# Performance work log

Measured on AMD Instinct MI355X. Metric: run time of the kernel, lower is better.

The kernel has to match this reference:

```python
import jax, jax.numpy as jnp
import numpy as np

H, D = 4, 64              # heads, per-head channels
NT, NC, NF = 20000, 200000, 40000  # table / column / fk_node counts
E_HC, E_BT, E_IS, E_PT = 200000, 200000, 80000, 80000


def _gatv2(x_src, x_dst, src, dst, Wl, Wr, att, b, n_dst):
    """PyG GATv2Conv (concat=True, negative_slope=0.2, no self loops)."""
    xl = (x_src @ Wl).reshape(-1, H, D)              # [Ns,H,D]
    xr = (x_dst @ Wr).reshape(-1, H, D)              # [Nd,H,D]
    e = jax.nn.leaky_relu(xl[src] + xr[dst], 0.2)    # [E,H,D]
    logit = jnp.einsum('ehd,hd->eh', e, att)         # [E,H]
    m = jax.ops.segment_max(logit, dst, num_segments=n_dst)
    z = jnp.exp(logit - m[dst])
    den = jax.ops.segment_sum(z, dst, num_segments=n_dst)
    alpha = z / den[dst]                             # softmax per dst node
    msg = xl[src] * alpha[:, :, None]                # [E,H,D]
    out = jax.ops.segment_sum(msg, dst, num_segments=n_dst)
    return out.reshape(n_dst, H * D) + b


def setup_inputs() -> dict:
    key = jax.random.key(0)
    ks = jax.random.split(key, 24)
    Fin, Fh, Fo = 256, H * D, 256
    f = lambda k, s: jax.random.normal(k, s, jnp.float32) * 0.05
    ri = lambda k, n, hi: jax.random.randint(k, (n,), 0, hi, jnp.int32)
    return dict(
        x_table=jax.random.normal(ks[0], (NT, Fin), jnp.float32),
        x_column=jax.random.normal(ks[1], (NC, Fin), jnp.float32),
        x_fk=jax.random.normal(ks[2], (NF, Fin), jnp.float32),
        lin_w=f(ks[3], (3, Fin, D)), lin_b=f(ks[4], (3, D)),
        out_w=f(ks[5], (3, Fh, Fo)), out_b=f(ks[6], (3, Fo)),
        Wl0=f(ks[7], (4, D, Fh)), Wr0=f(ks[8], (4, D, Fh)),
        att0=f(ks[9], (4, H, D)), b0=f(ks[10], (4, Fh)),
        Wl1=f(ks[11], (4, Fh, Fh)), Wr1=f(ks[12], (4, Fh, Fh)),
        att1=f(ks[13], (4, H, D)), b1=f(ks[14], (4, Fh)),
        src_hc=ri(ks[15], E_HC, NT), dst_hc=ri(ks[16], E_HC, NC),
        src_bt=ri(ks[17], E_BT, NC), dst_bt=ri(ks[18], E_BT, NT),
        src_is=ri(ks[19], E_IS, NC), dst_is=ri(ks[20], E_IS, NF),
        src_pt=ri(ks[21], E_PT, NF), dst_pt=ri(ks[22], E_PT, NC),
    )


def reference(x_table, x_column, x_fk, lin_w, lin_b, out_w, out_b,
              Wl0, Wr0, att0, b0, Wl1, Wr1, att1, b1,
              src_hc, dst_hc, src_bt, dst_bt, src_is, dst_is, src_pt, dst_pt):
    # per-type input projection + leaky_relu (slope 0.01)
    xt = jax.nn.leaky_relu(x_table @ lin_w[0] + lin_b[0], 0.01)
    xc = jax.nn.leaky_relu(x_column @ lin_w[1] + lin_b[1], 0.01)
    xf = jax.nn.leaky_relu(x_fk @ lin_w[2] + lin_b[2], 0.01)
    for Wl, Wr, att, b in ((Wl0, Wr0, att0, b0), (Wl1, Wr1, att1, b1)):
        o_hc = _gatv2(xt, xc, src_hc, dst_hc, Wl[0], Wr[0], att[0], b[0], NC)
        o_bt = _gatv2(xc, xt, src_bt, dst_bt, Wl[1], Wr[1], att[1], b[1], NT)
        o_is = _gatv2(xc, xf, src_is, dst_is, Wl[2], Wr[2], att[2], b[2], NF)
        o_pt = _gatv2(xf, xc, src_pt, dst_pt, Wl[3], Wr[3], att[3], b[3], NC)
        xt = jax.nn.elu(o_bt)                  # single edge type -> mean = itself
        xc = jax.nn.elu(0.5 * (o_hc + o_pt))   # HeteroConv aggr='mean'
        xf = jax.nn.elu(o_is)
    return (xt @ out_w[0] + out_b[0],
            xc @ out_w[1] + out_b[1],
            xf @ out_w[2] + out_b[2])
```

## Files before the change

### kernel.cpp

```cpp
#include <hip/hip_runtime.h>
#include <stdint.h>

typedef unsigned short ushort_t;
typedef unsigned int uint32;

#define NT 20000
#define NC 200000
#define NF 40000
#define E_HC 200000
#define E_BT 200000
#define E_IS 80000
#define E_PT 80000
#define FDIM 256
#define NHEAD 4
#define DHEAD 64

typedef _Float16 __attribute__((ext_vector_type(8))) half8;
typedef __attribute__((ext_vector_type(4))) float f32x4;

__device__ __forceinline__ ushort_t f2h(float f) {
    _Float16 h = (_Float16)f;
    ushort_t v;
    __builtin_memcpy(&v, &h, 2);
    return v;
}
__device__ __forceinline__ float h2f_u(ushort_t v) {
    _Float16 h;
    __builtin_memcpy(&h, &v, 2);
    return (float)h;
}
__device__ __forceinline__ float hlo(uint32 u) { return h2f_u((ushort_t)(u & 0xffffu)); }
__device__ __forceinline__ float hhi(uint32 u) { return h2f_u((ushort_t)(u >> 16)); }
__device__ __forceinline__ float finclamp(float v) {
    return fminf(fmaxf(v, -1e30f), 1e30f);
}

union U16x8 { ushort_t u[8]; uint4 q; };

__global__ void pack_layer_k(const float* __restrict__ Wl, const float* __restrict__ Wr,
                             ushort_t* __restrict__ ct, ushort_t* __restrict__ cc,
                             ushort_t* __restrict__ cf, int K) {
    int i = blockIdx.x * 256 + threadIdx.x;
    int per = K * 256;
    if (i >= 8 * per) return;
    int s = i / per, r = i - s * per;
    int k = r >> 8, n = r & 255;
    const float* src; ushort_t* dst; int col;
    switch (s) {
        case 0: src = Wl + 0 * per; dst = ct; col = n;        break;
        case 1: src = Wr + 1 * per; dst = ct; col = 256 + n;  break;
        case 2: src = Wr + 0 * per; dst = cc; col = n;        break;
        case 3: src = Wl + 1 * per; dst = cc; col = 256 + n;  break;
        case 4: src = Wl + 2 * per; dst = cc; col = 512 + n;  break;
        case 5: src = Wr + 3 * per; dst = cc; col = 768 + n;  break;
        case 6: src = Wr + 2 * per; dst = cf; col = n;        break;
        default: src = Wl + 3 * per; dst = cf; col = 256 + n; break;
    }
    dst[(size_t)col * K + k] = f2h(src[(size_t)k * 256 + n]);
}

__global__ void pack_out_k(const float* __restrict__ W, ushort_t* __restrict__ Wt) {
    int i = blockIdx.x * 256 + threadIdx.x;
    if (i >= 3 * 65536) return;
    int t = i >> 16, r = i & 65535;
    int k = r >> 8, n = r & 255;
    Wt[(size_t)t * 65536 + n * 256 + k] = f2h(W[(size_t)t * 65536 + k * 256 + n]);
}

__global__ void pack_lin_k(const float* __restrict__ W, ushort_t* __restrict__ Wt) {
    int i = blockIdx.x * 256 + threadIdx.x;
    if (i >= 3 * 16384) return;
    int t = i >> 14, r = i & 16383;
    int k = r >> 6, n = r & 63;
    Wt[(size_t)t * 16384 + n * 256 + k] = f2h(W[(size_t)t * 16384 + k * 64 + n]);
}

template<int CT>
__global__ __launch_bounds__(256) void gemm_mfma_k(
    const ushort_t* __restrict__ A, const ushort_t* __restrict__ Wt,
    const float* __restrict__ bias, void* __restrict__ Cv,
    int M, int N, int K)
{
    __shared__ __align__(16) ushort_t As[128][32];
    __shared__ __align__(16) ushort_t Bs[128][32];
    const int t = threadIdx.x;
    const int lane = t & 63;
    const int w = t >> 6;
    const int wr = (w >> 1) * 64, wc = (w & 1) * 64;
    const int m0 = blockIdx.x * 128;
    const int n0 = blockIdx.y * 128;
    const int lm = lane & 15, g = lane >> 4;

    f32x4 acc[4][4];
#pragma unroll
    for (int mi = 0; mi < 4; mi++)
#pragma unroll
        for (int ni = 0; ni < 4; ni++) acc[mi][ni] = (f32x4){0.f, 0.f, 0.f, 0.f};

    const int sr = t >> 1;
    const int ss = (t & 1) * 2;
    const int sw = (sr >> 1) & 3;

    for (int k0 = 0; k0 < K; k0 += 32) {
        {
            int row = m0 + sr;
            uint4 q0 = make_uint4(0u, 0u, 0u, 0u), q1 = q0;
            if (row < M) {
                const uint4* p = reinterpret_cast<const uint4*>(
                    A + (size_t)row * K + k0 + ss * 8);
                q0 = p[0]; q1 = p[1];
            }
            *reinterpret_cast<uint4*>(&As[sr][((ss + 0) ^ sw) * 8]) = q0;
            *reinterpret_cast<uint4*>(&As[sr][((ss + 1) ^ sw) * 8]) = q1;
        }
        {
            const uint4* p = reinterpret_cast<const uint4*>(
                Wt + (size_t)(n0 + sr) * K + k0 + ss * 8);
            uint4 q0 = p[0], q1 = p[1];
            *reinterpret_cast<uint4*>(&Bs[sr][((ss + 0) ^ sw) * 8]) = q0;
            *reinterpret_cast<uint4*>(&Bs[sr][((ss + 1) ^ sw) * 8]) = q1;
        }
        __syncthreads();
        half8 af[4], bf[4];
#pragma unroll
        for (int mi = 0; mi < 4; mi++) {
            int row = wr + mi * 16 + lm;
            af[mi] = *reinterpret_cast<const half8*>(
                &As[row][(g ^ ((row >> 1) & 3)) * 8]);
        }
#pragma unroll
        for (int ni = 0; ni < 4; ni++) {
            int row = wc + ni * 16 + lm;
            bf[ni] = *reinterpret_cast<const half8*>(
                &Bs[row][(g ^ ((row >> 1) & 3)) * 8]);
        }
#pragma unroll
        for (int mi = 0; mi < 4; mi++)
#pragma unroll
            for (int ni = 0; ni < 4; ni++)
                acc[mi][ni] = __builtin_amdgcn_mfma_f32_16x16x32_f16(
                    af[mi], bf[ni], acc[mi][ni], 0, 0, 0);
        __syncthreads();
    }

#pragma unroll
    for (int mi = 0; mi < 4; mi++) {
#pragma unroll
        for (int j = 0; j < 4; j++) {
            int row = m0 + wr + mi * 16 + g * 4 + j;
            if (row >= M) continue;
#pragma unroll
            for (int ni = 0; ni < 4; ni++) {
                int col = n0 + wc + ni * 16 + lm;
                float v = acc[mi][ni][j];
                if (bias) v += bias[col];
                v = finclamp(v);
                if (CT == 0) {
                    ((float*)Cv)[(size_t)row * N + col] = v;
                } else {
                    ((ushort_t*)Cv)[(size_t)row * N + col] = f2h(v);
                }
            }
        }
    }
}

__global__ __launch_bounds__(256) void gemm_in_k(
    const float* __restrict__ A, const ushort_t* __restrict__ Wt,
    const float* __restrict__ bias, ushort_t* __restrict__ C, int M, int K)
{
    __shared__ __align__(16) ushort_t As[128][32];
    __shared__ __align__(16) ushort_t Bs[64][32];
    const int t = threadIdx.x;
    const int lane = t & 63;
    const int w = t >> 6;
    const int m0 = blockIdx.x * 128;
    const int lm = lane & 15, g = lane >> 4;

    f32x4 acc[2][4];
#pragma unroll
    for (int mi = 0; mi < 2; mi++)
#pragma unroll
        for (int ni = 0; ni < 4; ni++) acc[mi][ni] = (f32x4){0.f, 0.f, 0.f, 0.f};

    const int sr = t >> 1;
    const int ss = (t & 1) * 2;
    const int sw = (sr >> 1) & 3;
    const int br = t >> 2;
    const int bs = t & 3;
    const int bw = (br >> 1) & 3;

    for (int k0 = 0; k0 < K; k0 += 32) {
        {
            int row = m0 + sr;
            U16x8 a, b;
            if (row < M) {
                const float4* p = reinterpret_cast<const float4*>(
                    A + (size_t)row * K + k0 + (t & 1) * 16);
                float4 q0 = p[0], q1 = p[1], q2 = p[2], q3 = p[3];
                a.u[0] = f2h(q0.x); a.u[1] = f2h(q0.y); a.u[2] = f2h(q0.z); a.u[3] = f2h(q0.w);
                a.u[4] = f2h(q1.x); a.u[5] = f2h(q1.y); a.u[6] = f2h(q1.z); a.u[7] = f2h(q1.w);
                b.u[0] = f2h(q2.x); b.u[1] = f2h(q2.y); b.u[2] = f2h(q2.z); b.u[3] = f2h(q2.w);
                b.u[4] = f2h(q3.x); b.u[5] = f2h(q3.y); b.u[6] = f2h(q3.z); b.u[7] = f2h(q3.w);
            } else {
                a.q = make_uint4(0u, 0u, 0u, 0u); b.q = a.q;
            }
            *reinterpret_cast<uint4*>(&As[sr][((ss + 0) ^ sw) * 8]) = a.q;
            *reinterpret_cast<uint4*>(&As[sr][((ss + 1) ^ sw) * 8]) = b.q;
        }
        {
            uint4 q = *reinterpret_cast<const uint4*>(
                Wt + (size_t)br * K + k0 + bs * 8);
            *reinterpret_cast<uint4*>(&Bs[br][(bs ^ bw) * 8]) = q;
        }
        __syncthreads();
        half8 af[2], bf[4];
#pragma unroll
        for (int mi = 0; mi < 2; mi++) {
            int row = w * 32 + mi * 16 + lm;
            af[mi] = *reinterpret_cast<const half8*>(
                &As[row][(g ^ ((row >> 1) & 3)) * 8]);
        }
#pragma unroll
        for (int ni = 0; ni < 4; ni++) {
            int row = ni * 16 + lm;
            bf[ni] = *reinterpret_cast<const half8*>(
                &Bs[row][(g ^ ((row >> 1) & 3)) * 8]);
        }
#pragma unroll
        for (int mi = 0; mi < 2; mi++)
#pragma unroll
            for (int ni = 0; ni < 4; ni++)
                acc[mi][ni] = __builtin_amdgcn_mfma_f32_16x16x32_f16(
                    af[mi], bf[ni], acc[mi][ni], 0, 0, 0);
        __syncthreads();
    }

#pragma unroll
    for (int mi = 0; mi < 2; mi++) {
#pragma unroll
        for (int j = 0; j < 4; j++) {
            int row = m0 + w * 32 + mi * 16 + g * 4 + j;
            if (row >= M) continue;
#pragma unroll
            for (int ni = 0; ni < 4; ni++) {
                int col = ni * 16 + lm;
                float v = acc[mi][ni][j] + bias[col];
                v = (v > 0.f) ? v : 0.01f * v;
                C[(size_t)row * 64 + col] = f2h(finclamp(v));
            }
        }
    }
}

__global__ void zero2_k(int* __restrict__ a, int* __restrict__ b, int n) {
    int i = blockIdx.x * 256 + threadIdx.x;
    if (i < n) { a[i] = 0; b[i] = 0; }
}

__global__ void hist_k(const int* __restrict__ dst, int* __restrict__ cnt, int E) {
    int e = blockIdx.x * 256 + threadIdx.x;
    if (e < E) atomicAdd(&cnt[dst[e]], 1);
}

__global__ __launch_bounds__(1024) void scan_blk_k(const int* __restrict__ cnt,
                                                   int* __restrict__ off,
                                                   int* __restrict__ bsum, int n) {
    __shared__ int wsum[16];
    int t = threadIdx.x, lane = t & 63, w = t >> 6;
    int i = blockIdx.x * 4096 + t * 4;
    int v[4];
#pragma unroll
    for (int k = 0; k < 4; k++) v[k] = (i + k < n) ? cnt[i + k] : 0;
    int ts = v[0] + v[1] + v[2] + v[3];
    int x = ts;
#pragma unroll
    for (int sh = 1; sh < 64; sh <<= 1) {
        int y = __shfl_up(x, sh);
        if (lane >= sh) x += y;
    }
    if (lane == 63) wsum[w] = x;
    __syncthreads();
    int wbase = 0;
    for (int k = 0; k < w; k++) wbase += wsum[k];
    int excl = wbase + (x - ts);
#pragma unroll
    for (int k = 0; k < 4; k++) {
        if (i + k < n) off[i + k] = excl;
        excl += v[k];
    }
    if (t == 1023) bsum[blockIdx.x] = wbase + x;
}

__global__ void scan_top_k(int* __restrict__ bsum, int* __restrict__ off,
                           int n, int nb) {
    int lane = threadIdx.x;
    int v = (lane < nb) ? bsum[lane] : 0;
    int x = v;
#pragma unroll
    for (int sh = 1; sh < 64; sh <<= 1) {
        int y = __shfl_up(x, sh);
        if (lane >= sh) x += y;
    }
    if (lane < nb) bsum[lane] = x - v;
    if (lane == 63) off[n] = x;
}

__global__ void scan_fix_k(int* __restrict__ off, const int* __restrict__ bsum, int n) {
    int i = blockIdx.x * 256 + threadIdx.x;
    if (i < n) off[i] += bsum[i >> 12];
}

__global__ void permsrc_k(const int* __restrict__ dst, const int* __restrict__ src,
                          const int* __restrict__ off, int* __restrict__ cur,
                          int* __restrict__ ssrc, int E) {
    int e = blockIdx.x * 256 + threadIdx.x;
    if (e >= E) return;
    int d = dst[e];
    int slot = atomicAdd(&cur[d], 1);
    ssrc[off[d] + slot] = src[e];
}

__device__ __forceinline__ void gat_accum(
    const ushort_t* __restrict__ xl, int ldl,
    const ushort_t* __restrict__ xr, int ldr,
    const float* __restrict__ att, const int* __restrict__ off,
    const int* __restrict__ ssrc, int d, int f,
    float& o0, float& o1, float& o2, float& o3)
{
    int j0 = off[d], j1 = off[d + 1];
    if (j0 == j1) return;
    float4 qa = *reinterpret_cast<const float4*>(att + f);
    uint2 qr = *reinterpret_cast<const uint2*>(xr + (size_t)d * ldr + f);
    float r0 = hlo(qr.x), r1 = hhi(qr.x), r2 = hlo(qr.y), r3 = hhi(qr.y);
    float m = -1e30f, den = 0.f;
    float a0 = 0.f, a1 = 0.f, a2 = 0.f, a3 = 0.f;
    for (int j = j0; j < j1; ++j) {
        int s = ssrc[j];
        uint2 ql = *reinterpret_cast<const uint2*>(xl + (size_t)s * ldl + f);
        float l0 = hlo(ql.x), l1 = hhi(ql.x), l2 = hlo(ql.y), l3 = hhi(ql.y);
        float v0 = l0 + r0, v1 = l1 + r1, v2 = l2 + r2, v3 = l3 + r3;
        v0 = (v0 > 0.f) ? v0 : 0.2f * v0;
        v1 = (v1 > 0.f) ? v1 : 0.2f * v1;
        v2 = (v2 > 0.f) ? v2 : 0.2f * v2;
        v3 = (v3 > 0.f) ? v3 : 0.2f * v3;
        float lg = qa.x * v0 + qa.y * v1 + qa.z * v2 + qa.w * v3;
        lg += __shfl_xor(lg, 1);
        lg += __shfl_xor(lg, 2);
        lg += __shfl_xor(lg, 4);
        lg += __shfl_xor(lg, 8);
        float mn = fmaxf(m, lg);
        float sc = expf(m - mn);
        float z  = expf(lg - mn);
        den = den * sc + z;
        a0 = a0 * sc + z * l0;
        a1 = a1 * sc + z * l1;
        a2 = a2 * sc + z * l2;
        a3 = a3 * sc + z * l3;
        m = mn;
    }
    float inv = (den > 0.f) ? 1.f / den : 0.f;
    o0 += finclamp(a0 * inv);
    o1 += finclamp(a1 * inv);
    o2 += finclamp(a2 * inv);
    o3 += finclamp(a3 * inv);
}

__global__ __launch_bounds__(256) void gat_gather2_k(
    const ushort_t* __restrict__ xl1, int ldl1,
    const ushort_t* __restrict__ xr1, int ldr1,
    const float* __restrict__ att1, const int* __restrict__ off1,
    const int* __restrict__ ssrc1,
    const ushort_t* __restrict__ xl2, int ldl2,
    const ushort_t* __restrict__ xr2, int ldr2,
    const float* __restrict__ att2, const int* __restrict__ off2,
    const int* __restrict__ ssrc2,
    const float* __restrict__ b1, const float* __restrict__ b2,
    float scale, ushort_t* __restrict__ xout, int Nd)
{
    int d = blockIdx.x * 4 + (threadIdx.x >> 6);
    if (d >= Nd) return;
    int lane = threadIdx.x & 63;
    int f = lane * 4;
    float o0 = 0.f, o1 = 0.f, o2 = 0.f, o3 = 0.f;
    gat_accum(xl1, ldl1, xr1, ldr1, att1, off1, ssrc1, d, f, o0, o1, o2, o3);
    if (off2) gat_accum(xl2, ldl2, xr2, ldr2, att2, off2, ssrc2, d, f, o0, o1, o2, o3);
    float4 bv = *reinterpret_cast<const float4*>(b1 + f);
    o0 += bv.x; o1 += bv.y; o2 += bv.z; o3 += bv.w;
    if (b2) {
        float4 b2v = *reinterpret_cast<const float4*>(b2 + f);
        o0 += b2v.x; o1 += b2v.y; o2 += b2v.z; o3 += b2v.w;
    }
    o0 *= scale; o1 *= scale; o2 *= scale; o3 *= scale;
    o0 = (o0 > 0.f) ? o0 : (expf(o0) - 1.f);
    o1 = (o1 > 0.f) ? o1 : (expf(o1) - 1.f);
    o2 = (o2 > 0.f) ? o2 : (expf(o2) - 1.f);
    o3 = (o3 > 0.f) ? o3 : (expf(o3) - 1.f);
    uint32 lo = ((uint32)f2h(finclamp(o1)) << 16) | (uint32)f2h(finclamp(o0));
    uint32 hi = ((uint32)f2h(finclamp(o3)) << 16) | (uint32)f2h(finclamp(o2));
    *reinterpret_cast<uint2*>(xout + (size_t)d * FDIM + f) = make_uint2(lo, hi);
}

extern "C" void kernel_launch(void* const* d_in, const int* in_sizes, int n_in,
                              void* d_out, int out_size, void* d_ws, size_t ws_size,
                              hipStream_t stream) {
    (void)in_sizes; (void)n_in; (void)out_size;
    const float* x_table = (const float*)d_in[0];
    const float* x_column = (const float*)d_in[1];
    const float* x_fk = (const float*)d_in[2];
    const float* lin_w = (const float*)d_in[3];
    const float* lin_b = (const float*)d_in[4];
    const float* out_w = (const float*)d_in[5];
    const float* out_b = (const float*)d_in[6];
    const float* Wl0 = (const float*)d_in[7];
    const float* Wr0 = (const float*)d_in[8];
    const float* att0 = (const float*)d_in[9];
    const float* b0 = (const float*)d_in[10];
    const float* Wl1 = (const float*)d_in[11];
    const float* Wr1 = (const float*)d_in[12];
    const float* att1 = (const float*)d_in[13];
    const float* b1 = (const float*)d_in[14];
    const int* src_hc = (const int*)d_in[15];
    const int* dst_hc = (const int*)d_in[16];
    const int* src_bt = (const int*)d_in[17];
    const int* dst_bt = (const int*)d_in[18];
    const int* src_is = (const int*)d_in[19];
    const int* dst_is = (const int*)d_in[20];
    const int* src_pt = (const int*)d_in[21];
    const int* dst_pt = (const int*)d_in[22];
    float* out = (float*)d_out;

    char* p = (char*)d_ws;
    auto alloc = [&](size_t bytes) -> char* {
        char* r = p;
        p += (bytes + 255) & ~(size_t)255;
        return r;
    };
    ushort_t* xt = (ushort_t*)alloc((size_t)NT * FDIM * 2);
    ushort_t* xc = (ushort_t*)alloc((size_t)NC * FDIM * 2);
    ushort_t* xf = (ushort_t*)alloc((size_t)NF * FDIM * 2);
    ushort_t* pt_buf = (ushort_t*)alloc((size_t)NT * 512 * 2);
    ushort_t* pc_buf = (ushort_t*)alloc((size_t)NC * 1024 * 2);
    ushort_t* pf_buf = (ushort_t*)alloc((size_t)NF * 512 * 2);
    int* off_hc = (int*)alloc((size_t)(NC + 1) * 4);
    int* off_bt = (int*)alloc((size_t)(NT + 1) * 4);
    int* off_is = (int*)alloc((size_t)(NF + 1) * 4);
    int* off_pt = (int*)alloc((size_t)(NC + 1) * 4);
    int* ssrc_hc = (int*)alloc((size_t)E_HC * 4);
    int* ssrc_bt = (int*)alloc((size_t)E_BT * 4);
    int* ssrc_is = (int*)alloc((size_t)E_IS * 4);
    int* ssrc_pt = (int*)alloc((size_t)E_PT * 4);
    int* cnt = (int*)alloc((size_t)NC * 4);
    int* cur = (int*)alloc((size_t)NC * 4);
    int* bsum = (int*)alloc((size_t)64 * 4);
    ushort_t* wcat_t0 = (ushort_t*)alloc((size_t)512 * 64 * 2);
    ushort_t* wcat_c0 = (ushort_t*)alloc((size_t)1024 * 64 * 2);
    ushort_t* wcat_f0 = (ushort_t*)alloc((size_t)512 * 64 * 2);
    ushort_t* wcat_t1 = (ushort_t*)alloc((size_t)512 * 256 * 2);
    ushort_t* wcat_c1 = (ushort_t*)alloc((size_t)1024 * 256 * 2);
    ushort_t* wcat_f1 = (ushort_t*)alloc((size_t)512 * 256 * 2);
    ushort_t* owt = (ushort_t*)alloc((size_t)3 * 65536 * 2);
    ushort_t* lint = (ushort_t*)alloc((size_t)3 * 16384 * 2);
    if ((size_t)(p - (char*)d_ws) > ws_size) return;

    hipLaunchKernelGGL(pack_layer_k, dim3((8 * 64 * 256 + 255) / 256), dim3(256), 0,
                       stream, Wl0, Wr0, wcat_t0, wcat_c0, wcat_f0, 64);
    hipLaunchKernelGGL(pack_layer_k, dim3((8 * 256 * 256 + 255) / 256), dim3(256), 0,
                       stream, Wl1, Wr1, wcat_t1, wcat_c1, wcat_f1, 256);
    hipLaunchKernelGGL(pack_out_k, dim3((3 * 65536 + 255) / 256), dim3(256), 0,
                       stream, out_w, owt);
    hipLaunchKernelGGL(pack_lin_k, dim3((3 * 16384 + 255) / 256), dim3(256), 0,
                       stream, lin_w, lint);

    auto build_csr = [&](const int* dst, const int* src, int E, int Nd,
                         int* off, int* ssrc) {
        int nb = (Nd + 4095) / 4096;
        hipLaunchKernelGGL(zero2_k, dim3((Nd + 255) / 256), dim3(256), 0, stream,
                           cnt, cur, Nd);
        hipLaunchKernelGGL(hist_k, dim3((E + 255) / 256), dim3(256), 0, stream,
                           dst, cnt, E);
        hipLaunchKernelGGL(scan_blk_k, dim3(nb), dim3(1024), 0, stream,
                           cnt, off, bsum, Nd);
        hipLaunchKernelGGL(scan_top_k, dim3(1), dim3(64), 0, stream,
                           bsum, off, Nd, nb);
        hipLaunchKernelGGL(scan_fix_k, dim3((Nd + 255) / 256), dim3(256), 0, stream,
                           off, bsum, Nd);
        hipLaunchKernelGGL(permsrc_k, dim3((E + 255) / 256), dim3(256), 0, stream,
                           dst, src, off, cur, ssrc, E);
    };
    build_csr(dst_hc, src_hc, E_HC, NC, off_hc, ssrc_hc);
    build_csr(dst_bt, src_bt, E_BT, NT, off_bt, ssrc_bt);
    build_csr(dst_is, src_is, E_IS, NF, off_is, ssrc_is);
    build_csr(dst_pt, src_pt, E_PT, NC, off_pt, ssrc_pt);

    hipLaunchKernelGGL(gemm_in_k, dim3((NT + 127) / 128), dim3(256), 0, stream,
                       x_table, lint + 0 * 16384, lin_b + 0 * 64, xt, NT, 256);
    hipLaunchKernelGGL(gemm_in_k, dim3((NC + 127) / 128), dim3(256), 0, stream,
                       x_column, lint + 1 * 16384, lin_b + 1 * 64, xc, NC, 256);
    hipLaunchKernelGGL(gemm_in_k, dim3((NF + 127) / 128), dim3(256), 0, stream,
                       x_fk, lint + 2 * 16384, lin_b + 2 * 64, xf, NF, 256);

    auto gemm_cat = [&](const ushort_t* A, const ushort_t* Wt, ushort_t* C,
                        int M, int N, int K) {
        hipLaunchKernelGGL((gemm_mfma_k<1>), dim3((M + 127) / 128, N / 128),
                           dim3(256), 0, stream, A, Wt, (const float*)nullptr,
                           (void*)C, M, N, K);
    };

    for (int l = 0; l < 2; l++) {
        const ushort_t* wt_t = l ? wcat_t1 : wcat_t0;
        const ushort_t* wt_c = l ? wcat_c1 : wcat_c0;
        const ushort_t* wt_f = l ? wcat_f1 : wcat_f0;
        const float* att = l ? att1 : att0;
        const float* bb = l ? b1 : b0;
        int Kd = l ? 256 : 64;

        gemm_cat(xt, wt_t, pt_buf, NT, 512, Kd);
        gemm_cat(xc, wt_c, pc_buf, NC, 1024, Kd);
        gemm_cat(xf, wt_f, pf_buf, NF, 512, Kd);

        hipLaunchKernelGGL(gat_gather2_k, dim3((NT + 3) / 4), dim3(256), 0, stream,
                           pc_buf + 256, 1024, pt_buf + 256, 512,
                           att + 1 * FDIM, off_bt, ssrc_bt,
                           (const ushort_t*)nullptr, 0, (const ushort_t*)nullptr, 0,
                           (const float*)nullptr, (const int*)nullptr,
                           (const int*)nullptr,
                           bb + 1 * FDIM, (const float*)nullptr, 1.0f, xt, NT);
        hipLaunchKernelGGL(gat_gather2_k, dim3((NF + 3) / 4), dim3(256), 0, stream,
                           pc_buf + 512, 1024, pf_buf + 0, 512,
                           att + 2 * FDIM, off_is, ssrc_is,
                           (const ushort_t*)nullptr, 0, (const ushort_t*)nullptr, 0,
                           (const float*)nullptr, (const int*)nullptr,
                           (const int*)nullptr,
                           bb + 2 * FDIM, (const float*)nullptr, 1.0f, xf, NF);
        hipLaunchKernelGGL(gat_gather2_k, dim3((NC + 3) / 4), dim3(256), 0, stream,
                           pt_buf + 0, 512, pc_buf + 0, 1024,
                           att + 0 * FDIM, off_hc, ssrc_hc,
                           pf_buf + 256, 512, pc_buf + 768, 1024,
                           att + 3 * FDIM, off_pt, ssrc_pt,
                           bb + 0 * FDIM, bb + 3 * FDIM, 0.5f, xc, NC);
    }

    hipLaunchKernelGGL((gemm_mfma_k<0>), dim3((NT + 127) / 128, 2), dim3(256), 0,
                       stream, xt, owt + 0 * 65536, out_b + 0 * 256,
                       (void*)out, NT, 256, 256);
    hipLaunchKernelGGL((gemm_mfma_k<0>), dim3((NC + 127) / 128, 2), dim3(256), 0,
                       stream, xc, owt + 1 * 65536, out_b + 1 * 256,
                       (void*)(out + (size_t)NT * FDIM), NC, 256, 256);
    hipLaunchKernelGGL((gemm_mfma_k<0>), dim3((NF + 127) / 128, 2), dim3(256), 0,
                       stream, xf, owt + 2 * 65536, out_b + 2 * 256,
                       (void*)(out + (size_t)(NT + NC) * FDIM), NF, 256, 256);
}
```

Measured before the change: 1.649 ms.

## Keep A tile resident in LDS across N blocks and merge CSR builds

The GEMM kernel now loads the full 128xK A tile into LDS once, then loops over several 128-column output blocks while streaming only the weight tiles. This avoids re-reading the activation matrix for every output column block, which matters most for the 1024-wide column projection. Separately, the four per-relation CSR builds are merged into one concatenated histogram/scan/permute pass, cutting the number of kernel launches. The resident tile uses up to 72KB of LDS for K=256, which may reduce occupancy, and each block now does serial work over its N blocks.

New measurement: 1.752 ms. 6.2% more time.

```diff
diff --git a/kernel.cpp b/kernel.cpp
--- a/kernel.cpp
+++ b/kernel.cpp
@@ -14,6 +14,16 @@
 #define FDIM 256
 #define NHEAD 4
 #define DHEAD 64
+
+#define B_HC 0
+#define B_BT (NC)
+#define B_IS (NC + NT)
+#define B_PT (NC + NT + NF)
+#define NTOT (2 * NC + NT + NF)
+#define EB_BT (E_HC)
+#define EB_IS (E_HC + E_BT)
+#define EB_PT (E_HC + E_BT + E_IS)
+#define ETOT  (E_HC + E_BT + E_IS + E_PT)
 
 typedef _Float16 __attribute__((ext_vector_type(8))) half8;
 typedef __attribute__((ext_vector_type(4))) float f32x4;
@@ -75,90 +85,94 @@
     Wt[(size_t)t * 16384 + n * 256 + k] = f2h(W[(size_t)t * 16384 + k * 64 + n]);
 }
 
-template<int CT>
-__global__ __launch_bounds__(256) void gemm_mfma_k(
+template<int CT, int K>
+__global__ __launch_bounds__(256) void gemm_ares_k(
     const ushort_t* __restrict__ A, const ushort_t* __restrict__ Wt,
     const float* __restrict__ bias, void* __restrict__ Cv,
-    int M, int N, int K)
+    int M, int N, int NBY)
 {
-    __shared__ __align__(16) ushort_t As[128][32];
-    __shared__ __align__(16) ushort_t Bs[128][32];
+    extern __shared__ __align__(16) ushort_t lds[];
+    ushort_t* As = lds;
+    ushort_t* Bs = lds + 128 * K;
     const int t = threadIdx.x;
     const int lane = t & 63;
     const int w = t >> 6;
     const int wr = (w >> 1) * 64, wc = (w & 1) * 64;
     const int m0 = blockIdx.x * 128;
-    const int n0 = blockIdx.y * 128;
     const int lm = lane & 15, g = lane >> 4;
-
-    f32x4 acc[4][4];
-#pragma unroll
-    for (int mi = 0; mi < 4; mi++)
-#pragma unroll
-        for (int ni = 0; ni < 4; ni++) acc[mi][ni] = (f32x4){0.f, 0.f, 0.f, 0.f};
-
+    constexpr int KS = K >> 3;
+
+    for (int c = t; c < 128 * KS; c += 256) {
+        int row = c / KS, slot = c - row * KS;
+        int grow = m0 + row;
+        uint4 q = make_uint4(0u, 0u, 0u, 0u);
+        if (grow < M)
+            q = *reinterpret_cast<const uint4*>(A + (size_t)grow * K + slot * 8);
+        *reinterpret_cast<uint4*>(&As[row * K + (slot ^ (row & 7)) * 8]) = q;
+    }
     const int sr = t >> 1;
     const int ss = (t & 1) * 2;
     const int sw = (sr >> 1) & 3;
-
-    for (int k0 = 0; k0 < K; k0 += 32) {
-        {
-            int row = m0 + sr;
-            uint4 q0 = make_uint4(0u, 0u, 0u, 0u), q1 = q0;
-            if (row < M) {
-                const uint4* p = reinterpret_cast<const uint4*>(
-                    A + (size_t)row * K + k0 + ss * 8);
-                q0 = p[0]; q1 = p[1];
+    __syncthreads();
+
+    for (int nb = 0; nb < NBY; ++nb) {
+        const int n0 = (blockIdx.y * NBY + nb) << 7;
+        f32x4 acc[4][4];
+#pragma unroll
+        for (int mi = 0; mi < 4; mi++)
+#pragma unroll
+            for (int ni = 0; ni < 4; ni++) acc[mi][ni] = (f32x4){0.f, 0.f, 0.f, 0.f};
+
+#pragma unroll
+        for (int kk = 0; kk < K / 32; ++kk) {
+            const int k0 = kk * 32;
+            {
+                const uint4* pb = reinterpret_cast<const uint4*>(
+                    Wt + (size_t)(n0 + sr) * K + k0 + ss * 8);
+                uint4 b0 = pb[0], b1 = pb[1];
+                *reinterpret_cast<uint4*>(&Bs[sr * 32 + ((ss + 0) ^ sw) * 8]) = b0;
+                *reinterpret_cast<uint4*>(&Bs[sr * 32 + ((ss + 1) ^ sw) * 8]) = b1;
             }
-            *reinterpret_cast<uint4*>(&As[sr][((ss + 0) ^ sw) * 8]) = q0;
-            *reinterpret_cast<uint4*>(&As[sr][((ss + 1) ^ sw) * 8]) = q1;
-        }
-        {
-            const uint4* p = reinterpret_cast<const uint4*>(
-                Wt + (size_t)(n0 + sr) * K + k0 + ss * 8);
-            uint4 q0 = p[0], q1 = p[1];
-            *reinterpret_cast<uint4*>(&Bs[sr][((ss + 0) ^ sw) * 8]) = q0;
-            *reinterpret_cast<uint4*>(&Bs[sr][((ss + 1) ^ sw) * 8]) = q1;
-        }
-        __syncthreads();
-        half8 af[4], bf[4];
+            __syncthreads();
+            half8 af[4], bf[4];
+#pragma unroll
+            for (int mi = 0; mi < 4; mi++) {
+                int row = wr + mi * 16 + lm;
+                af[mi] = *reinterpret_cast<const half8*>(
+                    &As[row * K + ((kk * 4 + g) ^ (row & 7)) * 8]);
+            }
+#pragma unroll
+            for (int ni = 0; ni < 4; ni++) {
+                int row = wc + ni * 16 + lm;
+                bf[ni] = *reinterpret_cast<const half8*>(
+                    &Bs[row * 32 + (g ^ ((row >> 1) & 3)) * 8]);
+            }
+#pragma unroll
+            for (int mi = 0; mi < 4; mi++)
+#pragma unroll
+                for (int ni = 0; ni < 4; ni++)
+                    acc[mi][ni] = __builtin_amdgcn_mfma_f32_16x16x32_f16(
+                        af[mi], bf[ni], acc[mi][ni], 0, 0, 0);
+            __syncthreads();
+        }
+
 #pragma unroll
         for (int mi = 0; mi < 4; mi++) {
-            int row = wr + mi * 16 + lm;
-            af[mi] = *reinterpret_cast<const half8*>(
-                &As[row][(g ^ ((row >> 1) & 3)) * 8]);
-        }
-#pragma unroll
-        for (int ni = 0; ni < 4; ni++) {
-            int row = wc + ni * 16 + lm;
-            bf[ni] = *reinterpret_cast<const half8*>(
-                &Bs[row][(g ^ ((row >> 1) & 3)) * 8]);
-        }
-#pragma unroll
-        for (int mi = 0; mi < 4; mi++)
-#pragma unroll
-            for (int ni = 0; ni < 4; ni++)
-                acc[mi][ni] = __builtin_amdgcn_mfma_f32_16x16x32_f16(
-                    af[mi], bf[ni], acc[mi][ni], 0, 0, 0);
-        __syncthreads();
-    }
-
-#pragma unroll
-    for (int mi = 0; mi < 4; mi++) {
-#pragma unroll
-        for (int j = 0; j < 4; j++) {
-            int row = m0 + wr + mi * 16 + g * 4 + j;
-            if (row >= M) continue;
-#pragma unroll
-            for (int ni = 0; ni < 4; ni++) {
-                int col = n0 + wc + ni * 16 + lm;
-                float v = acc[mi][ni][j];
-                if (bias) v += bias[col];
-                v = finclamp(v);
-                if (CT == 0) {
-                    ((float*)Cv)[(size_t)row * N + col] = v;
-                } else {
-                    ((ushort_t*)Cv)[(size_t)row * N + col] = f2h(v);
+#pragma unroll
+            for (int j = 0; j < 4; j++) {
+                int row = m0 + wr + mi * 16 + g * 4 + j;
+                if (row >= M) continue;
+#pragma unroll
+                for (int ni = 0; ni < 4; ni++) {
+                    int col = n0 + wc + ni * 16 + lm;
+                    float v = acc[mi][ni][j];
+                    if (bias) v += bias[col];
+                    v = finclamp(v);
+                    if (CT == 0) {
+                        ((float*)Cv)[(size_t)row * N + col] = v;
+                    } else {
+                        ((ushort_t*)Cv)[(size_t)row * N + col] = f2h(v);
+                    }
                 }
             }
         }
@@ -253,26 +267,36 @@
     }
 }
 
-__global__ void zero2_k(int* __restrict__ a, int* __restrict__ b, int n) {
+__global__ void zero_cc_k(int* __restrict__ cnt, int* __restrict__ cur) {
     int i = blockIdx.x * 256 + threadIdx.x;
-    if (i < n) { a[i] = 0; b[i] = 0; }
-}
-
-__global__ void hist_k(const int* __restrict__ dst, int* __restrict__ cnt, int E) {
+    if (i < NTOT) { cnt[i] = 0; cur[i] = 0; }
+}
+
+__global__ void hist4_k(const int* __restrict__ dhc, const int* __restrict__ dbt,
+                        const int* __restrict__ dis, const int* __restrict__ dpt,
+                        int* __restrict__ cnt) {
     int e = blockIdx.x * 256 + threadIdx.x;
-    if (e < E) atomicAdd(&cnt[dst[e]], 1);
-}
-
-__global__ __launch_bounds__(1024) void scan_blk_k(const int* __restrict__ cnt,
-                                                   int* __restrict__ off,
-                                                   int* __restrict__ bsum, int n) {
+    if (e >= ETOT) return;
+    int idx;
+    if (e < EB_BT)      idx = B_HC + dhc[e];
+    else if (e < EB_IS) idx = B_BT + dbt[e - EB_BT];
+    else if (e < EB_PT) idx = B_IS + dis[e - EB_IS];
+    else                idx = B_PT + dpt[e - EB_PT];
+    atomicAdd(&cnt[idx], 1);
+}
+
+__global__ __launch_bounds__(1024) void scan_blk8_k(const int* __restrict__ cnt,
+                                                    int* __restrict__ off,
+                                                    int* __restrict__ bsum, int n) {
     __shared__ int wsum[16];
     int t = threadIdx.x, lane = t & 63, w = t >> 6;
-    int i = blockIdx.x * 4096 + t * 4;
-    int v[4];
-#pragma unroll
-    for (int k = 0; k < 4; k++) v[k] = (i + k < n) ? cnt[i + k] : 0;
-    int ts = v[0] + v[1] + v[2] + v[3];
+    int i = blockIdx.x * 8192 + t * 8;
+    int v[8];
+#pragma unroll
+    for (int k = 0; k < 8; k++) v[k] = (i + k < n) ? cnt[i + k] : 0;
+    int ts = 0;
+#pragma unroll
+    for (int k = 0; k < 8; k++) ts += v[k];
     int x = ts;
 #pragma unroll
     for (int sh = 1; sh < 64; sh <<= 1) {
@@ -285,7 +309,7 @@
     for (int k = 0; k < w; k++) wbase += wsum[k];
     int excl = wbase + (x - ts);
 #pragma unroll
-    for (int k = 0; k < 4; k++) {
+    for (int k = 0; k < 8; k++) {
         if (i + k < n) off[i + k] = excl;
         excl += v[k];
     }
@@ -306,19 +330,26 @@
     if (lane == 63) off[n] = x;
 }
 
-__global__ void scan_fix_k(int* __restrict__ off, const int* __restrict__ bsum, int n) {
+__global__ void scan_fix8_k(int* __restrict__ off, const int* __restrict__ bsum, int n) {
     int i = blockIdx.x * 256 + threadIdx.x;
-    if (i < n) off[i] += bsum[i >> 12];
-}
-
-__global__ void permsrc_k(const int* __restrict__ dst, const int* __restrict__ src,
-                          const int* __restrict__ off, int* __restrict__ cur,
-                          int* __restrict__ ssrc, int E) {
+    if (i < n) off[i] += bsum[i >> 13];
+}
+
+__global__ void perm4_k(const int* __restrict__ shc, const int* __restrict__ dhc,
+                        const int* __restrict__ sbt, const int* __restrict__ dbt,
+                        const int* __restrict__ sis, const int* __restrict__ dis,
+                        const int* __restrict__ spt, const int* __restrict__ dpt,
+                        const int* __restrict__ off, int* __restrict__ cur,
+                        int* __restrict__ ssrc) {
     int e = blockIdx.x * 256 + threadIdx.x;
-    if (e >= E) return;
-    int d = dst[e];
-    int slot = atomicAdd(&cur[d], 1);
-    ssrc[off[d] + slot] = src[e];
+    if (e >= ETOT) return;
+    int idx, sv;
+    if (e < EB_BT)      { idx = B_HC + dhc[e];            sv = shc[e]; }
+    else if (e < EB_IS) { int l = e - EB_BT; idx = B_BT + dbt[l]; sv = sbt[l]; }
+    else if (e < EB_PT) { int l = e - EB_IS; idx = B_IS + dis[l]; sv = sis[l]; }
+    else                { int l = e - EB_PT; idx = B_PT + dpt[l]; sv = spt[l]; }
+    int slot = atomicAdd(&cur[idx], 1);
+    ssrc[off[idx] + slot] = sv;
 }
 
 __device__ __forceinline__ void gat_accum(
@@ -430,6 +461,19 @@
     const int* dst_pt = (const int*)d_in[22];
     float* out = (float*)d_out;
 
+    static bool attr_done = false;
+    if (!attr_done) {
+        int sz256 = 128 * 256 * 2 + 128 * 32 * 2;
+        int sz64  = 128 * 64 * 2 + 128 * 32 * 2;
+        hipFuncSetAttribute(reinterpret_cast<const void*>(&gemm_ares_k<1, 256>),
+                            hipFuncAttributeMaxDynamicSharedMemorySize, sz256);
+        hipFuncSetAttribute(reinterpret_cast<const void*>(&gemm_ares_k<0, 256>),
+                            hipFuncAttributeMaxDynamicSharedMemorySize, sz256);
+        hipFuncSetAttribute(reinterpret_cast<const void*>(&gemm_ares_k<1, 64>),
+                            hipFuncAttributeMaxDynamicSharedMemorySize, sz64);
+        attr_done = true;
+    }
+
     char* p = (char*)d_ws;
     auto alloc = [&](size_t bytes) -> char* {
         char* r = p;
@@ -442,16 +486,10 @@
     ushort_t* pt_buf = (ushort_t*)alloc((size_t)NT * 512 * 2);
     ushort_t* pc_buf = (ushort_t*)alloc((size_t)NC * 1024 * 2);
     ushort_t* pf_buf = (ushort_t*)alloc((size_t)NF * 512 * 2);
-    int* off_hc = (int*)alloc((size_t)(NC + 1) * 4);
-    int* off_bt = (int*)alloc((size_t)(NT + 1) * 4);
-    int* off_is = (int*)alloc((size_t)(NF + 1) * 4);
-    int* off_pt = (int*)alloc((size_t)(NC + 1) * 4);
-    int* ssrc_hc = (int*)alloc((size_t)E_HC * 4);
-    int* ssrc_bt = (int*)alloc((size_t)E_BT * 4);
-    int* ssrc_is = (int*)alloc((size_t)E_IS * 4);
-    int* ssrc_pt = (int*)alloc((size_t)E_PT * 4);
-    int* cnt = (int*)alloc((size_t)NC * 4);
-    int* cur = (int*)alloc((size_t)NC * 4);
+    int* off_cat = (int*)alloc((size_t)(NTOT + 1) * 4);
+    int* ssrc_cat = (int*)alloc((size_t)ETOT * 4);
+    int* cnt = (int*)alloc((size_t)NTOT * 4);
+    int* cur = (int*)alloc((size_t)NTOT * 4);
     int* bsum = (int*)alloc((size_t)64 * 4);
     ushort_t* wcat_t0 = (ushort_t*)alloc((size_t)512 * 64 * 2);
     ushort_t* wcat_c0 = (ushort_t*)alloc((size_t)1024 * 64 * 2);
@@ -472,26 +510,22 @@
     hipLaunchKernelGGL(pack_lin_k, dim3((3 * 16384 + 255) / 256), dim3(256), 0,
                        stream, lin_w, lint);
 
-    auto build_csr = [&](const int* dst, const int* src, int E, int Nd,
-                         int* off, int* ssrc) {
-        int nb = (Nd + 4095) / 4096;
-        hipLaunchKernelGGL(zero2_k, dim3((Nd + 255) / 256), dim3(256), 0, stream,
-                           cnt, cur, Nd);
-        hipLaunchKernelGGL(hist_k, dim3((E + 255) / 256), dim3(256), 0, stream,
-                           dst, cnt, E);
-        hipLaunchKernelGGL(scan_blk_k, dim3(nb), dim3(1024), 0, stream,
-                           cnt, off, bsum, Nd);
+    {
+        int nb = (NTOT + 8191) / 8192;
+        hipLaunchKernelGGL(zero_cc_k, dim3((NTOT + 255) / 256), dim3(256), 0, stream,
+                           cnt, cur);
+        hipLaunchKernelGGL(hist4_k, dim3((ETOT + 255) / 256), dim3(256), 0, stream,
+                           dst_hc, dst_bt, dst_is, dst_pt, cnt);
+        hipLaunchKernelGGL(scan_blk8_k, dim3(nb), dim3(1024), 0, stream,
+                           cnt, off_cat, bsum, NTOT);
         hipLaunchKernelGGL(scan_top_k, dim3(1), dim3(64), 0, stream,
-                           bsum, off, Nd, nb);
-        hipLaunchKernelGGL(scan_fix_k, dim3((Nd + 255) / 256), dim3(256), 0, stream,
-                           off, bsum, Nd);
-        hipLaunchKernelGGL(permsrc_k, dim3((E + 255) / 256), dim3(256), 0, stream,
-                           dst, src, off, cur, ssrc, E);
-    };
-    build_csr(dst_hc, src_hc, E_HC, NC, off_hc, ssrc_hc);
-    build_csr(dst_bt, src_bt, E_BT, NT, off_bt, ssrc_bt);
-    build_csr(dst_is, src_is, E_IS, NF, off_is, ssrc_is);
-    build_csr(dst_pt, src_pt, E_PT, NC, off_pt, ssrc_pt);
+                           bsum, off_cat, NTOT, nb);
+        hipLaunchKernelGGL(scan_fix8_k, dim3((NTOT + 255) / 256), dim3(256), 0, stream,
+                           off_cat, bsum, NTOT);
+        hipLaunchKernelGGL(perm4_k, dim3((ETOT + 255) / 256), dim3(256), 0, stream,
+                           src_hc, dst_hc, src_bt, dst_bt, src_is, dst_is,
+                           src_pt, dst_pt, off_cat, cur, ssrc_cat);
+    }
 
     hipLaunchKernelGGL(gemm_in_k, dim3((NT + 127) / 128), dim3(256), 0, stream,
                        x_table, lint + 0 * 16384, lin_b + 0 * 64, xt, NT, 256);
@@ -500,11 +534,26 @@
     hipLaunchKernelGGL(gemm_in_k, dim3((NF + 127) / 128), dim3(256), 0, stream,
                        x_fk, lint + 2 * 16384, lin_b + 2 * 64, xf, NF, 256);
 
-    auto gemm_cat = [&](const ushort_t* A, const ushort_t* Wt, ushort_t* C,
-                        int M, int N, int K) {
-        hipLaunchKernelGGL((gemm_mfma_k<1>), dim3((M + 127) / 128, N / 128),
-                           dim3(256), 0, stream, A, Wt, (const float*)nullptr,
-                           (void*)C, M, N, K);
+    auto ares16 = [&](const ushort_t* A, const ushort_t* Wt, ushort_t* C,
+                      int M, int N, int K, int gy) {
+        int nby = (N >> 7) / gy;
+        dim3 grid((M + 127) / 128, gy);
+        if (K == 256) {
+            int sz = 128 * 256 * 2 + 128 * 32 * 2;
+            hipLaunchKernelGGL((gemm_ares_k<1, 256>), grid, dim3(256), sz, stream,
+                               A, Wt, (const float*)nullptr, (void*)C, M, N, nby);
+        } else {
+            int sz = 128 * 64 * 2 + 128 * 32 * 2;
+            hipLaunchKernelGGL((gemm_ares_k<1, 64>), grid, dim3(256), sz, stream,
+                               A, Wt, (const float*)nullptr, (void*)C, M, N, nby);
+        }
+    };
+    auto ares32 = [&](const ushort_t* A, const ushort_t* Wt, const float* bias,
+                      float* C, int M, int N, int gy) {
+        int nby = (N >> 7) / gy;
+        int sz = 128 * 256 * 2 + 128 * 32 * 2;
+        hipLaunchKernelGGL((gemm_ares_k<0, 256>), dim3((M + 127) / 128, gy),
+                           dim3(256), sz, stream, A, Wt, bias, (void*)C, M, N, nby);
     };
 
     for (int l = 0; l < 2; l++) {
@@ -515,39 +564,34 @@
         const float* bb = l ? b1 : b0;
         int Kd = l ? 256 : 64;
 
-        gemm_cat(xt, wt_t, pt_buf, NT, 512, Kd);
-        gemm_cat(xc, wt_c, pc_buf, NC, 1024, Kd);
-        gemm_cat(xf, wt_f, pf_buf, NF, 512, Kd);
+        ares16(xt, wt_t, pt_buf, NT, 512, Kd, 4);
+        ares16(xc, wt_c, pc_buf, NC, 1024, Kd, 1);
+        ares16(xf, wt_f, pf_buf, NF, 512, Kd, 2);
 
         hipLaunchKernelGGL(gat_gather2_k, dim3((NT + 3) / 4), dim3(256), 0, stream,
                            pc_buf + 256, 1024, pt_buf + 256, 512,
-                           att + 1 * FDIM, off_bt, ssrc_bt,
+                           att + 1 * FDIM, off_cat + B_BT, ssrc_cat,
                            (const ushort_t*)nullptr, 0, (const ushort_t*)nullptr, 0,
                            (const float*)nullptr, (const int*)nullptr,
                            (const int*)nullptr,
                            bb + 1 * FDIM, (const float*)nullptr, 1.0f, xt, NT);
         hipLaunchKernelGGL(gat_gather2_k, dim3((NF + 3) / 4), dim3(256), 0, stream,
                            pc_buf + 512, 1024, pf_buf + 0, 512,
-                           att + 2 * FDIM, off_is, ssrc_is,
+                           att + 2 * FDIM, off_cat + B_IS, ssrc_cat,
                            (const ushort_t*)nullptr, 0, (const ushort_t*)nullptr, 0,
                            (const float*)nullptr, (const int*)nullptr,
                            (const int*)nullptr,
                            bb + 2 * FDIM, (const float*)nullptr, 1.0f, xf, NF);
         hipLaunchKernelGGL(gat_gather2_k, dim3((NC + 3) / 4), dim3(256), 0, stream,
                            pt_buf + 0, 512, pc_buf + 0, 1024,
-                           att + 0 * FDIM, off_hc, ssrc_hc,
+                           att + 0 * FDIM, off_cat + B_HC, ssrc_cat,
                            pf_buf + 256, 512, pc_buf + 768, 1024,
-                           att + 3 * FDIM, off_pt, ssrc_pt,
+                           att + 3 * FDIM, off_cat + B_PT, ssrc_cat,
                            bb + 0 * FDIM, bb + 3 * FDIM, 0.5f, xc, NC);
     }
 
-    hipLaunchKernelGGL((gemm_mfma_k<0>), dim3((NT + 127) / 128, 2), dim3(256), 0,
-                       stream, xt, owt + 0 * 65536, out_b + 0 * 256,
-                       (void*)out, NT, 256, 256);
-    hipLaunchKernelGGL((gemm_mfma_k<0>), dim3((NC + 127) / 128, 2), dim3(256), 0,
-                       stream, xc, owt + 1 * 65536, out_b + 1 * 256,
-                       (void*)(out + (size_t)NT * FDIM), NC, 256, 256);
-    hipLaunchKernelGGL((gemm_mfma_k<0>), dim3((NF + 127) / 128, 2), dim3(256), 0,
-                       stream, xf, owt + 2 * 65536, out_b + 2 * 256,
-                       (void*)(out + (size_t)(NT + NC) * FDIM), NF, 256, 256);
-}
+    ares32(xt, owt + 0 * 65536, out_b + 0 * 256, out, NT, 256, 2);
+    ares32(xc, owt + 1 * 65536, out_b + 1 * 256, out + (size_t)NT * FDIM, NC, 256, 1);
+    ares32(xf, owt + 2 * 65536, out_b + 2 * 256, out + (size_t)(NT + NC) * FDIM,
+           NF, 256, 2);
+}
```
